# Kernel optimization log

Measured on AMD Instinct MI355X. Metric: run time of the kernel, lower is better.

## Reference

```python
import jax, jax.numpy as jnp
import numpy as np

B, LQ, LK, D = 8, 1024, 4096, 1024


def setup_inputs() -> dict:
    key = jax.random.key(0)
    k1, k2, k3, k4, k5, k6 = jax.random.split(key, 6)
    s = 1.0 / np.sqrt(D)
    return {
        "T": jax.random.normal(k1, (B, LQ, D), dtype=jnp.float32),
        "S": jax.random.normal(k2, (B, LK, D), dtype=jnp.float32),
        "Wq": jax.random.uniform(k3, (D, D), jnp.float32, -s, s),
        "Wk": jax.random.uniform(k4, (D, D), jnp.float32, -s, s),
        "Wv": jax.random.uniform(k5, (D, D), jnp.float32, -s, s),
        "Wo": jax.random.uniform(k6, (D, D), jnp.float32, -s, s),
    }


def reference(T, S, Wq, Wk, Wv, Wo):
    # Linear layers: y = x @ W.T (torch nn.Linear convention), bias=False
    q = jnp.einsum('bqd,ed->bqe', T, Wq)          # [B, LQ, D]
    k = jnp.einsum('bkd,ed->bke', S, Wk)          # [B, LK, D]
    v = jnp.einsum('bkd,ed->bke', S, Wv)          # [B, LK, D]
    scale = jnp.asarray(D, q.dtype) ** -0.5        # hidden_dim ** -0.5 (single head)
    attn = jnp.einsum('bqe,bke->bqk', q, k) * scale  # [B, LQ, LK]
    attn = jax.nn.softmax(attn, axis=-1)
    out = jnp.einsum('bqk,bke->bqe', attn, v)      # [B, LQ, D]
    return jnp.einsum('bqe,fe->bqf', out, Wo)      # output projection
```

## Files before the change

kernel.cpp:

```cpp
#include <hip/hip_runtime.h>
#include <stdint.h>

typedef __bf16 bf16;
typedef __bf16 bf16x8 __attribute__((ext_vector_type(8)));
typedef float f32x4 __attribute__((ext_vector_type(4)));

__device__ __forceinline__ void gload_lds16(const void* g, void* l) {
    __builtin_amdgcn_global_load_lds(
        (const __attribute__((address_space(1))) unsigned int*)g,
        (__attribute__((address_space(3))) unsigned int*)l, 16, 0, 0);
}

#define BAR()    asm volatile("s_barrier" ::: "memory")
#define WAITV(N) asm volatile("s_waitcnt vmcnt(" #N ")" ::: "memory")

template<bool OUT_BF16>
__global__ __launch_bounds__(512, 2)
void gemm256(const bf16* __restrict__ A, const bf16* __restrict__ B,
             void* __restrict__ Cv, int K, int N,
             long batchA, long batchB, long batchC, float alpha,
             int nbx, int nby, int GC)
{
    __shared__ __align__(16) bf16 lds[2][4][8192];

    const int nwg  = gridDim.x;
    const int orig = blockIdx.x;
    const int q8   = nwg >> 3, r8 = nwg & 7;
    const int xcd  = orig & 7, lid = orig >> 3;
    const int p    = (xcd < r8 ? xcd * (q8 + 1) : r8 * (q8 + 1) + (xcd - r8) * q8) + lid;
    const int perb = nbx * nby;
    const int z    = p / perb;
    const int pb   = p - z * perb;
    const int sw   = nby * GC;
    const int st   = pb / sw;
    const int rem  = pb - st * sw;
    const int by   = rem / GC;
    const int bx   = st * GC + (rem - by * GC);

    const long rowb = (long)by << 8;
    const long colb = (long)bx << 8;

    const int t  = threadIdx.x;
    const int l  = t & 63;
    const int w  = t >> 6;
    const int wm = w >> 2;
    const int wn = w & 3;

    const int sL   = (t * 16) ^ (((t >> 3) & 3) << 4);
    const int srow = sL >> 6;
    const int sk   = (sL & 63) >> 1;
    const bf16* Ab = A + (long)z * batchA;
    const bf16* Bb = B + (long)z * batchB;
    const bf16* gA = Ab + (rowb + srow) * (long)K + sk;
    const bf16* gB = Bb + (colb + srow) * (long)K + sk;
    const long rstep = 128L * K;
    const int  d0 = t * 8, d1 = t * 8 + 4096;

    const int xl    = ((l >> 1) & 3) << 4;
    const int aBase = ((wm * 128 + (l & 15)) * 64 + ((l >> 4) << 4)) ^ xl;
    const int bBase = ((wn * 64  + (l & 15)) * 64 + ((l >> 4) << 4)) ^ xl;

    f32x4 acc[8][4] = {};
    bf16x8 av[4], bv[4];

#define STG(S, R, G, KOFF) do { \
    const bf16* _g = (G) + (KOFF); \
    gload_lds16(_g,         &lds[S][R][d0]); \
    gload_lds16(_g + rstep, &lds[S][R][d1]); \
  } while (0)

#define RD(S, R, OFF) (*(const bf16x8*)((const char*)&lds[S][R][0] + (OFF)))

#define MM(MB) \
    __builtin_amdgcn_s_setprio(1); \
    _Pragma("unroll") for (int mi = 0; mi < 4; ++mi) \
      _Pragma("unroll") for (int nj = 0; nj < 4; ++nj) \
        acc[MB + mi][nj] = __builtin_amdgcn_mfma_f32_16x16x32_bf16(av[mi], bv[nj], acc[MB + mi][nj], 0, 0, 0); \
    __builtin_amdgcn_s_setprio(0);

#define PH1(S, STGX) { \
    _Pragma("unroll") for (int nj = 0; nj < 4; ++nj) bv[nj] = RD(S, 2, bBase + nj * 1024); \
    _Pragma("unroll") for (int mi = 0; mi < 4; ++mi) av[mi] = RD(S, 0, aBase + mi * 1024); \
    STGX; BAR(); MM(0) BAR(); }

#define PH2(S, STGX) { \
    _Pragma("unroll") for (int mi = 0; mi < 4; ++mi) av[mi] = RD(S, 0, aBase + 4096 + mi * 1024); \
    STGX; BAR(); MM(4) BAR(); }

#define PH3(S, STGX) { \
    _Pragma("unroll") for (int nj = 0; nj < 4; ++nj) bv[nj] = RD(S, 3, bBase + nj * 1024); \
    _Pragma("unroll") for (int mi = 0; mi < 4; ++mi) av[mi] = RD(S, 1, aBase + mi * 1024); \
    STGX; BAR(); MM(0) BAR(); }

#define PH4(S, STGX, WT) { \
    _Pragma("unroll") for (int mi = 0; mi < 4; ++mi) av[mi] = RD(S, 1, aBase + 4096 + mi * 1024); \
    STGX; BAR(); MM(4) WT; BAR(); }

    STG(0, 0, gA, 0);
    STG(0, 1, gA, 32);
    STG(0, 2, gB, 0);
    STG(0, 3, gB, 32);
    STG(1, 2, gB, 64);
    STG(1, 0, gA, 64);
    STG(1, 3, gB, 96);
    WAITV(6);
    BAR();

    const int NI = K >> 7;
    for (int i = 0; i < NI - 1; ++i) {
        const int kb = i << 7;
        const int kn = kb + 128;
        PH1(0, STG(1, 1, gA, kb + 96));
        PH2(0, STG(0, 2, gB, kn));
        PH3(0, STG(0, 0, gA, kn));
        PH4(0, STG(0, 3, gB, kn + 32), WAITV(6));
        PH1(1, STG(0, 1, gA, kn + 32));
        PH2(1, STG(1, 2, gB, kn + 64));
        PH3(1, STG(1, 0, gA, kn + 64));
        PH4(1, STG(1, 3, gB, kn + 96), WAITV(6));
    }
    {
        const int kb = (NI - 1) << 7;
        PH1(0, STG(1, 1, gA, kb + 96));
        PH2(0, );
        PH3(0, );
        PH4(0, , WAITV(0));
        PH1(1, );
        PH2(1, );
        PH3(1, );
        PH4(1, , );
    }
#undef STG
#undef RD
#undef MM
#undef PH1
#undef PH2
#undef PH3
#undef PH4

    const int r0  = (l >> 4) << 2;
    const long cb0 = colb + wn * 64 + (l & 15);
    const long rb0 = rowb + wm * 128 + r0;
#pragma unroll
    for (int mf = 0; mf < 8; ++mf)
#pragma unroll
      for (int nj = 0; nj < 4; ++nj) {
        const long col = cb0 + nj * 16;
#pragma unroll
        for (int r = 0; r < 4; ++r) {
            const long row = rb0 + mf * 16 + r;
            const float vv = acc[mf][nj][r] * alpha;
            const long idx = (long)z * batchC + row * (long)N + col;
            if constexpr (OUT_BF16) ((bf16*)Cv)[idx] = (bf16)vv;
            else                    ((float*)Cv)[idx] = vv;
        }
      }
}

__global__ void cvt_bf16(const float* __restrict__ in, bf16* __restrict__ out, long n8)
{
    const long stride = (long)gridDim.x * 256;
    for (long i = (long)blockIdx.x * 256 + threadIdx.x; i < n8; i += stride) {
        const float4* p = (const float4*)in + i * 2;
        float4 a = p[0], b = p[1];
        union { bf16 h[8]; uint4 u; } o;
        o.h[0] = (bf16)a.x; o.h[1] = (bf16)a.y; o.h[2] = (bf16)a.z; o.h[3] = (bf16)a.w;
        o.h[4] = (bf16)b.x; o.h[5] = (bf16)b.y; o.h[6] = (bf16)b.z; o.h[7] = (bf16)b.w;
        ((uint4*)out)[i] = o.u;
    }
}

__global__ __launch_bounds__(256)
void transpose_v(const bf16* __restrict__ v, bf16* __restrict__ vT)
{
    __shared__ bf16 tile[64 * 72];
    const int b  = blockIdx.z;
    const int j0 = blockIdx.x * 64;
    const int e0 = blockIdx.y * 64;
    const int t  = threadIdx.x;
#pragma unroll
    for (int it = 0; it < 2; ++it) {
        int idx = it * 256 + t;
        int jj  = idx >> 3;
        int e8  = (idx & 7) << 3;
        uint4 d = *(const uint4*)&v[((long)b * 4096 + j0 + jj) * 1024 + e0 + e8];
        *(uint4*)&tile[jj * 72 + e8] = d;
    }
    __syncthreads();
#pragma unroll
    for (int it = 0; it < 2; ++it) {
        int idx = it * 256 + t;
        int ee  = idx >> 3;
        int j8  = (idx & 7) << 3;
        union { bf16 h[8]; uint4 u; } o;
#pragma unroll
        for (int s = 0; s < 8; ++s) o.h[s] = tile[(j8 + s) * 72 + ee];
        *(uint4*)&vT[((long)b * 1024 + e0 + ee) * 4096 + j0 + j8] = o.u;
    }
}

__global__ __launch_bounds__(256)
void softmax_rows(bf16* __restrict__ P)
{
    const long base = (long)blockIdx.x * 4096;
    const int t = threadIdx.x;
    union U { uint4 u; bf16 h[8]; };
    U d0, d1;
    d0.u = *(const uint4*)&P[base + t * 8];
    d1.u = *(const uint4*)&P[base + 2048 + t * 8];
    float v[16];
#pragma unroll
    for (int i = 0; i < 8; ++i) { v[i] = (float)d0.h[i]; v[8 + i] = (float)d1.h[i]; }
    float mx = v[0];
#pragma unroll
    for (int i = 1; i < 16; ++i) mx = fmaxf(mx, v[i]);
    for (int o = 32; o; o >>= 1) mx = fmaxf(mx, __shfl_xor(mx, o));
    __shared__ float redm[4], reds[4];
    if ((t & 63) == 0) redm[t >> 6] = mx;
    __syncthreads();
    mx = fmaxf(fmaxf(redm[0], redm[1]), fmaxf(redm[2], redm[3]));
    float s = 0.f;
#pragma unroll
    for (int i = 0; i < 16; ++i) { v[i] = __expf(v[i] - mx); s += v[i]; }
    for (int o = 32; o; o >>= 1) s += __shfl_xor(s, o);
    if ((t & 63) == 0) reds[t >> 6] = s;
    __syncthreads();
    s = reds[0] + reds[1] + reds[2] + reds[3];
    const float inv = 1.f / s;
    U o0, o1;
#pragma unroll
    for (int i = 0; i < 8; ++i) {
        o0.h[i] = (bf16)(v[i] * inv);
        o1.h[i] = (bf16)(v[8 + i] * inv);
    }
    *(uint4*)&P[base + t * 8]        = o0.u;
    *(uint4*)&P[base + 2048 + t * 8] = o1.u;
}

extern "C" void kernel_launch(void* const* d_in, const int* in_sizes, int n_in,
                              void* d_out, int out_size, void* d_ws, size_t ws_size,
                              hipStream_t stream)
{
    (void)in_sizes; (void)n_in; (void)out_size; (void)ws_size;
    const float* T  = (const float*)d_in[0];
    const float* S  = (const float*)d_in[1];
    const float* Wq = (const float*)d_in[2];
    const float* Wk = (const float*)d_in[3];
    const float* Wv = (const float*)d_in[4];
    const float* Wo = (const float*)d_in[5];
    float* Y = (float*)d_out;
    char* ws = (char*)d_ws;

    bf16* Wqb = (bf16*)(ws + 0);
    bf16* Wkb = (bf16*)(ws + 2097152);
    bf16* Wvb = (bf16*)(ws + 4194304);
    bf16* Wob = (bf16*)(ws + 6291456);
    bf16* Tb  = (bf16*)(ws + 8388608);
    bf16* Ob  = Tb;
    bf16* Qb  = (bf16*)(ws + 25165824);
    bf16* Sb  = (bf16*)(ws + 41943040);
    bf16* VTb = Sb;
    bf16* Kb  = (bf16*)(ws + 109051904);
    bf16* Vb  = (bf16*)(ws + 176160768);
    bf16* Pb  = Vb;

    cvt_bf16<<<512,   256, 0, stream>>>(Wq, Wqb, 131072);
    cvt_bf16<<<512,   256, 0, stream>>>(Wk, Wkb, 131072);
    cvt_bf16<<<512,   256, 0, stream>>>(Wv, Wvb, 131072);
    cvt_bf16<<<512,   256, 0, stream>>>(Wo, Wob, 131072);
    cvt_bf16<<<4096,  256, 0, stream>>>(T, Tb, 1048576);
    cvt_bf16<<<16384, 256, 0, stream>>>(S, Sb, 4194304);

    gemm256<true><<<128, 512, 0, stream>>>(Tb, Wqb, Qb, 1024, 1024, 0, 0, 0, 1.f, 4, 32, 4);
    gemm256<true><<<512, 512, 0, stream>>>(Sb, Wkb, Kb, 1024, 1024, 0, 0, 0, 1.f, 4, 128, 4);
    gemm256<true><<<512, 512, 0, stream>>>(Sb, Wvb, Vb, 1024, 1024, 0, 0, 0, 1.f, 4, 128, 4);

    transpose_v<<<dim3(64, 16, 8), 256, 0, stream>>>(Vb, VTb);

    gemm256<true><<<512, 512, 0, stream>>>(Qb, Kb, Pb, 1024, 4096,
        1024L * 1024, 4096L * 1024, 1024L * 4096, 0.03125f, 16, 4, 4);

    softmax_rows<<<8192, 256, 0, stream>>>(Pb);

    gemm256<true><<<128, 512, 0, stream>>>(Pb, VTb, Ob, 4096, 1024,
        1024L * 4096, 1024L * 4096, 1024L * 1024, 1.f, 4, 4, 2);

    gemm256<false><<<128, 512, 0, stream>>>(Ob, Wob, Y, 1024, 1024, 0, 0, 0, 1.f, 4, 32, 4);
}
```

Baseline: 468.2 us.

## Stage GEMM epilogue through LDS and fuse V transpose into projection

The GEMM epilogue now writes bf16 results into shared memory and then stores 16-byte coalesced rows, instead of scattered 2-byte stores. A new mode writes the V projection already transposed, so the separate transpose kernel and its round trip through memory are removed. The workspace buffers are remapped and the P·V grouping parameter changes from 2 to 4. The cost is extra LDS traffic and two barriers per half-tile in the epilogue.

```diff
diff --git a/kernel.cpp b/kernel.cpp
--- a/kernel.cpp
+++ b/kernel.cpp
@@ -14,7 +14,7 @@
 #define BAR()    asm volatile("s_barrier" ::: "memory")
 #define WAITV(N) asm volatile("s_waitcnt vmcnt(" #N ")" ::: "memory")
 
-template<bool OUT_BF16>
+template<int OMODE>
 __global__ __launch_bounds__(512, 2)
 void gemm256(const bf16* __restrict__ A, const bf16* __restrict__ B,
              void* __restrict__ Cv, int K, int N,
@@ -138,23 +138,61 @@
 #undef PH3
 #undef PH4
 
-    const int r0  = (l >> 4) << 2;
-    const long cb0 = colb + wn * 64 + (l & 15);
-    const long rb0 = rowb + wm * 128 + r0;
-#pragma unroll
-    for (int mf = 0; mf < 8; ++mf)
-#pragma unroll
-      for (int nj = 0; nj < 4; ++nj) {
-        const long col = cb0 + nj * 16;
-#pragma unroll
-        for (int r = 0; r < 4; ++r) {
-            const long row = rb0 + mf * 16 + r;
-            const float vv = acc[mf][nj][r] * alpha;
-            const long idx = (long)z * batchC + row * (long)N + col;
-            if constexpr (OUT_BF16) ((bf16*)Cv)[idx] = (bf16)vv;
-            else                    ((float*)Cv)[idx] = vv;
+    const int r0 = (l >> 4) << 2;
+
+    if constexpr (OMODE == 2) {
+        const long cb0 = colb + wn * 64 + (l & 15);
+        const long rb0 = rowb + wm * 128 + r0;
+#pragma unroll
+        for (int mf = 0; mf < 8; ++mf)
+#pragma unroll
+          for (int nj = 0; nj < 4; ++nj) {
+            const long col = cb0 + nj * 16;
+#pragma unroll
+            for (int r = 0; r < 4; ++r) {
+                const long row = rb0 + mf * 16 + r;
+                ((float*)Cv)[(long)z * batchC + row * (long)N + col] = acc[mf][nj][r] * alpha;
+            }
+          }
+    } else {
+        bf16* epi = &lds[0][0][0];
+        const int rrow   = t >> 5;
+        const int cchunk = (t & 31) << 3;
+        const int myh = (OMODE == 0) ? wm : (wn >> 1);
+#pragma unroll
+        for (int h = 0; h < 2; ++h) {
+            if (myh == h) {
+#pragma unroll
+                for (int mf = 0; mf < 8; ++mf)
+#pragma unroll
+                  for (int nj = 0; nj < 4; ++nj)
+#pragma unroll
+                    for (int r = 0; r < 4; ++r) {
+                        const float v = acc[mf][nj][r] * alpha;
+                        int orow = wm * 128 + mf * 16 + r0 + r;
+                        int ocol = wn * 64 + nj * 16 + (l & 15);
+                        if (OMODE == 1) { int tmp = orow; orow = ocol; ocol = tmp; }
+                        epi[(orow - h * 128) * 280 + ocol] = (bf16)v;
+                    }
+            }
+            __syncthreads();
+#pragma unroll
+            for (int pp = 0; pp < 8; ++pp) {
+                const int lrow = pp * 16 + rrow;
+                const int row  = h * 128 + lrow;
+                uint4 d = *(const uint4*)&epi[lrow * 280 + cchunk];
+                if (OMODE == 0) {
+                    bf16* Cb = (bf16*)Cv + (long)z * batchC;
+                    *(uint4*)&Cb[(rowb + row) * (long)N + colb + cchunk] = d;
+                } else {
+                    const long zz  = rowb >> 12;
+                    const long lk0 = (rowb & 4095) + cchunk;
+                    *(uint4*)&((bf16*)Cv)[zz * 4194304L + (colb + row) * 4096L + lk0] = d;
+                }
+            }
+            __syncthreads();
         }
-      }
+    }
 }
 
 __global__ void cvt_bf16(const float* __restrict__ in, bf16* __restrict__ out, long n8)
@@ -167,35 +205,6 @@
         o.h[0] = (bf16)a.x; o.h[1] = (bf16)a.y; o.h[2] = (bf16)a.z; o.h[3] = (bf16)a.w;
         o.h[4] = (bf16)b.x; o.h[5] = (bf16)b.y; o.h[6] = (bf16)b.z; o.h[7] = (bf16)b.w;
         ((uint4*)out)[i] = o.u;
-    }
-}
-
-__global__ __launch_bounds__(256)
-void transpose_v(const bf16* __restrict__ v, bf16* __restrict__ vT)
-{
-    __shared__ bf16 tile[64 * 72];
-    const int b  = blockIdx.z;
-    const int j0 = blockIdx.x * 64;
-    const int e0 = blockIdx.y * 64;
-    const int t  = threadIdx.x;
-#pragma unroll
-    for (int it = 0; it < 2; ++it) {
-        int idx = it * 256 + t;
-        int jj  = idx >> 3;
-        int e8  = (idx & 7) << 3;
-        uint4 d = *(const uint4*)&v[((long)b * 4096 + j0 + jj) * 1024 + e0 + e8];
-        *(uint4*)&tile[jj * 72 + e8] = d;
-    }
-    __syncthreads();
-#pragma unroll
-    for (int it = 0; it < 2; ++it) {
-        int idx = it * 256 + t;
-        int ee  = idx >> 3;
-        int j8  = (idx & 7) << 3;
-        union { bf16 h[8]; uint4 u; } o;
-#pragma unroll
-        for (int s = 0; s < 8; ++s) o.h[s] = tile[(j8 + s) * 72 + ee];
-        *(uint4*)&vT[((long)b * 1024 + e0 + ee) * 4096 + j0 + j8] = o.u;
     }
 }
 
@@ -259,10 +268,9 @@
     bf16* Ob  = Tb;
     bf16* Qb  = (bf16*)(ws + 25165824);
     bf16* Sb  = (bf16*)(ws + 41943040);
-    bf16* VTb = Sb;
+    bf16* Pb  = Sb;
     bf16* Kb  = (bf16*)(ws + 109051904);
-    bf16* Vb  = (bf16*)(ws + 176160768);
-    bf16* Pb  = Vb;
+    bf16* VTb = (bf16*)(ws + 176160768);
 
     cvt_bf16<<<512,   256, 0, stream>>>(Wq, Wqb, 131072);
     cvt_bf16<<<512,   256, 0, stream>>>(Wk, Wkb, 131072);
@@ -271,19 +279,17 @@
     cvt_bf16<<<4096,  256, 0, stream>>>(T, Tb, 1048576);
     cvt_bf16<<<16384, 256, 0, stream>>>(S, Sb, 4194304);
 
-    gemm256<true><<<128, 512, 0, stream>>>(Tb, Wqb, Qb, 1024, 1024, 0, 0, 0, 1.f, 4, 32, 4);
-    gemm256<true><<<512, 512, 0, stream>>>(Sb, Wkb, Kb, 1024, 1024, 0, 0, 0, 1.f, 4, 128, 4);
-    gemm256<true><<<512, 512, 0, stream>>>(Sb, Wvb, Vb, 1024, 1024, 0, 0, 0, 1.f, 4, 128, 4);
-
-    transpose_v<<<dim3(64, 16, 8), 256, 0, stream>>>(Vb, VTb);
-
-    gemm256<true><<<512, 512, 0, stream>>>(Qb, Kb, Pb, 1024, 4096,
+    gemm256<0><<<128, 512, 0, stream>>>(Tb, Wqb, Qb, 1024, 1024, 0, 0, 0, 1.f, 4, 32, 4);
+    gemm256<0><<<512, 512, 0, stream>>>(Sb, Wkb, Kb, 1024, 1024, 0, 0, 0, 1.f, 4, 128, 4);
+    gemm256<1><<<512, 512, 0, stream>>>(Sb, Wvb, VTb, 1024, 1024, 0, 0, 0, 1.f, 4, 128, 4);
+
+    gemm256<0><<<512, 512, 0, stream>>>(Qb, Kb, Pb, 1024, 4096,
         1024L * 1024, 4096L * 1024, 1024L * 4096, 0.03125f, 16, 4, 4);
 
     softmax_rows<<<8192, 256, 0, stream>>>(Pb);
 
-    gemm256<true><<<128, 512, 0, stream>>>(Pb, VTb, Ob, 4096, 1024,
-        1024L * 4096, 1024L * 4096, 1024L * 1024, 1.f, 4, 4, 2);
-
-    gemm256<false><<<128, 512, 0, stream>>>(Ob, Wob, Y, 1024, 1024, 0, 0, 0, 1.f, 4, 32, 4);
-}
+    gemm256<0><<<128, 512, 0, stream>>>(Pb, VTb, Ob, 4096, 1024,
+        1024L * 4096, 1024L * 4096, 1024L * 1024, 1.f, 4, 4, 4);
+
+    gemm256<2><<<128, 512, 0, stream>>>(Ob, Wob, Y, 1024, 1024, 0, 0, 0, 1.f, 4, 32, 4);
+}
```

New measurement: 448.3 us. 4.3% less time.
